# Optimization experiments

Hardware: AMD Instinct MI355X
Metric: run time of the kernel (lower is better)

The kernel has to match this reference:

```python
import jax, jax.numpy as jnp
import numpy as np

DT = 0.5
T = 50

def rho(x):
    return jnp.clip(x, 0.0, 1.0)

def rhop(x):
    return ((x >= 0.0) & (x <= 1.0)).astype(x.dtype)

def setup_inputs() -> dict:
    key = jax.random.key(0)
    ks = jax.random.split(key, 8)
    B, OUT, H, IN = 16384, 10, 256, 784
    data = jax.random.uniform(ks[0], (B, IN), dtype=jnp.float32)
    s0 = jnp.zeros((B, OUT), jnp.float32)
    s1 = jnp.zeros((B, H), jnp.float32)
    s2 = jnp.zeros((B, H), jnp.float32)
    # nn.Linear weights: shape (out_features, in_features), y = x @ W.T + b
    def lin(k, o, i):
        bound = 1.0 / np.sqrt(i)
        kw, kb = jax.random.split(k)
        W = jax.random.uniform(kw, (o, i), jnp.float32, -bound, bound)
        b = jax.random.uniform(kb, (o,), jnp.float32, -bound, bound)
        return W, b
    W0, b0 = lin(ks[1], OUT, H)   # w[0]: Linear(H, OUT)
    W2, b2 = lin(ks[2], H, H)     # w[2]: Linear(H, H)
    W4, b4 = lin(ks[3], H, IN)    # w[-1]: Linear(IN, H)
    return {"data": data, "s0": s0, "s1": s1, "s2": s2,
            "W0": W0, "b0": b0, "W2": W2, "b2": b2, "W4": W4, "b4": b4}

def reference(data, s0, s1, s2, W0, b0, W2, b2, W4, b4):
    # method='nograd', beta=0: run T stepper iterations, clamp states to [0,1].
    rdata = rho(data)  # constant over time steps
    def step(s, _):
        s0, s1, s2 = s
        d0 = -s0 + rho(s1) @ W0.T + b0
        d1 = -s1 + rhop(s1) * (rho(s2) @ W2.T + b2 + rho(s0) @ W0)
        d2 = -s2 + rhop(s2) * (rdata @ W4.T + b4 + rho(s1) @ W2)
        s0 = jnp.clip(s0 + DT * d0, 0.0, 1.0)
        s1 = jnp.clip(s1 + DT * d1, 0.0, 1.0)
        s2 = jnp.clip(s2 + DT * d2, 0.0, 1.0)
        return (s0, s1, s2), None
    (s0, s1, s2), _ = jax.lax.scan(step, (s0, s1, s2), None, length=T)
    return (s0, s1, s2)
```

## Files before the change

kernel.cpp:

```cpp
#include <hip/hip_runtime.h>

typedef _Float16 f16;
typedef _Float16 f16x8 __attribute__((ext_vector_type(8)));
typedef _Float16 f16x4 __attribute__((ext_vector_type(4)));
typedef float f32x4 __attribute__((ext_vector_type(4)));

#define MFMA16(a, b, c) __builtin_amdgcn_mfma_f32_16x16x32_f16((a), (b), (c), 0, 0, 0)
#define CLAMP01(x) __builtin_amdgcn_fmed3f((x), 0.0f, 1.0f)

constexpr int BATCH = 16384;
constexpr int H     = 256;
constexpr int IN    = 784;
constexpr int OUT   = 10;
constexpr int TSTEP = 50;
constexpr int BM    = 64;
constexpr int NTHR  = 512;
constexpr int SROW  = 264;
constexpr int S0ROW = 40;
constexpr int DROW  = 808;
constexpr int BXROW = 268;
constexpr int W0TROW= 16;
constexpr int EROW  = 268;

constexpr int OFF_S1  = 0;
constexpr int OFF_S2  = OFF_S1 + BM * SROW;
constexpr int OFF_S0  = OFF_S2 + BM * SROW;
constexpr int OFF_W0N = OFF_S0 + BM * S0ROW;
constexpr int OFF_W0T = OFF_W0N + 16 * SROW;
constexpr int OFF_B2  = OFF_W0T + H * W0TROW;
constexpr int OFF_BX  = OFF_B2 + 2 * H;
constexpr int POOL_F16 = OFF_BX + 2 * BM * BXROW;

__global__ __launch_bounds__(NTHR, 2) void ep_step_kernel(
    const float* __restrict__ data, const float* __restrict__ s0_in,
    const float* __restrict__ s1_in, const float* __restrict__ s2_in,
    const float* __restrict__ W0, const float* __restrict__ b0,
    const float* __restrict__ W2, const float* __restrict__ b2,
    const float* __restrict__ W4, const float* __restrict__ b4,
    float* __restrict__ out)
{
    __shared__ __align__(16) f16 pool[POOL_F16];

    const int tid  = threadIdx.x;
    const int wave = tid >> 6;
    const int lane = tid & 63;
    const int q    = lane >> 4;
    const int l16  = lane & 15;
    const int m0   = blockIdx.x * BM;
    const bool isS1 = (wave >= 4);
    const int  dmt  = wave & 3;
    const int h0   = (wave & 3) * 64;
    const int hx   = wave * 32;

    float* const bx  = (float*)&pool[OFF_BX];
    float* const b2l = (float*)&pool[OFF_B2];

    for (int i = tid; i < BM * (DROW / 4); i += NTHR) {
        int m  = i / (DROW / 4);
        int k4 = (i % (DROW / 4)) * 4;
        f16x4 p = {(f16)0.f, (f16)0.f, (f16)0.f, (f16)0.f};
        if (k4 < IN) {
            f32x4 v = *(const f32x4*)(data + (size_t)(m0 + m) * IN + k4);
            #pragma unroll
            for (int j = 0; j < 4; ++j) p[j] = (f16)CLAMP01(v[j]);
        }
        *(f16x4*)&pool[m * DROW + k4] = p;
    }
    __syncthreads();

    f32x4 x2a[2][4] = {};
    for (int kk = 0; kk < 25; ++kk) {
        int kb = kk * 32 + q * 8;
        f16x8 bd[4];
        #pragma unroll
        for (int mt = 0; mt < 4; ++mt)
            bd[mt] = *(const f16x8*)&pool[(mt * 16 + l16) * DROW + kb];
        #pragma unroll
        for (int ht = 0; ht < 2; ++ht) {
            int h = hx + ht * 16 + l16;
            f16x8 wa4;
            if (kk < 24) {
                f32x4 u0 = *(const f32x4*)(W4 + (size_t)h * IN + kb);
                f32x4 u1 = *(const f32x4*)(W4 + (size_t)h * IN + kb + 4);
                #pragma unroll
                for (int j = 0; j < 4; ++j) { wa4[j] = (f16)u0[j]; wa4[j + 4] = (f16)u1[j]; }
            } else {
                #pragma unroll
                for (int j = 0; j < 8; ++j) {
                    int k = kb + j;
                    wa4[j] = (k < IN) ? (f16)W4[(size_t)h * IN + k] : (f16)0.f;
                }
            }
            #pragma unroll
            for (int mt = 0; mt < 4; ++mt)
                x2a[ht][mt] = MFMA16(wa4, bd[mt], x2a[ht][mt]);
        }
    }
    __syncthreads();

    #pragma unroll
    for (int ht = 0; ht < 2; ++ht)
        #pragma unroll
        for (int mt = 0; mt < 4; ++mt) {
            f32x4 v = x2a[ht][mt];
            #pragma unroll
            for (int r = 0; r < 4; ++r) v[r] = 0.5f * (v[r] + b4[hx + ht * 16 + q * 4 + r]);
            *(f32x4*)&bx[(mt * 16 + l16) * BXROW + hx + ht * 16 + q * 4] = v;
        }
    for (int i = tid; i < 16 * SROW; i += NTHR) {
        int o = i / SROW, k = i % SROW;
        pool[OFF_W0N + i] = (o < OUT && k < H) ? (f16)W0[o * H + k] : (f16)0.f;
    }
    for (int i = tid; i < H * W0TROW; i += NTHR) {
        int h = i / W0TROW, o = i % W0TROW;
        pool[OFF_W0T + i] = (o < OUT) ? (f16)W0[o * H + h] : (f16)0.f;
    }
    for (int i = tid; i < H; i += NTHR) b2l[i] = 0.5f * b2[i];
    for (int i = tid; i < BM * S0ROW; i += NTHR) pool[OFF_S0 + i] = (f16)0.f;
    __syncthreads();

    asm volatile("" ::: "memory");
    f16x8 w[4][8];
    if (!isS1) {
        #pragma unroll
        for (int ht = 0; ht < 4; ++ht) {
            int h = h0 + ht * 16 + l16;
            #pragma unroll
            for (int kk = 0; kk < 8; ++kk) {
                int kb = kk * 32 + q * 8;
                f16x8 wa;
                #pragma unroll
                for (int j = 0; j < 8; ++j) wa[j] = (f16)W2[(kb + j) * H + h];
                w[ht][kk] = wa;
            }
        }
    } else {
        #pragma unroll
        for (int ht = 0; ht < 4; ++ht) {
            int h = h0 + ht * 16 + l16;
            #pragma unroll
            for (int kk = 0; kk < 8; ++kk) {
                int kb = kk * 32 + q * 8;
                f32x4 u0 = *(const f32x4*)(W2 + h * H + kb);
                f32x4 u1 = *(const f32x4*)(W2 + h * H + kb + 4);
                f16x8 wb;
                #pragma unroll
                for (int j = 0; j < 4; ++j) { wb[j] = (f16)u0[j]; wb[j + 4] = (f16)u1[j]; }
                w[ht][kk] = wb;
            }
        }
    }
    f32x4 sm[4][4];
    const float* sin_p = isS1 ? s1_in : s2_in;
    #pragma unroll
    for (int ht = 0; ht < 4; ++ht)
        #pragma unroll
        for (int mt = 0; mt < 4; ++mt)
            sm[ht][mt] = *(const f32x4*)&sin_p[(size_t)(m0 + mt * 16 + l16) * H + h0 + ht * 16 + q * 4];
    f32x4 s0m = {0.f, 0.f, 0.f, 0.f}, b0h = {0.f, 0.f, 0.f, 0.f};
    if (!isS1) {
        #pragma unroll
        for (int r = 0; r < 4; ++r) {
            int o = q * 4 + r;
            if (o < OUT) {
                s0m[r] = s0_in[(size_t)(m0 + dmt * 16 + l16) * OUT + o];
                b0h[r] = 0.5f * b0[o];
            }
        }
    }

    auto writeback = [&]() {
        f16* ws = &pool[isS1 ? OFF_S1 : OFF_S2];
        #pragma unroll
        for (int ht = 0; ht < 4; ++ht) {
            int hb = h0 + ht * 16 + q * 4;
            #pragma unroll
            for (int mt = 0; mt < 4; ++mt) {
                f16x4 p;
                #pragma unroll
                for (int r = 0; r < 4; ++r) p[r] = (f16)sm[ht][mt][r];
                *(f16x4*)&ws[(mt * 16 + l16) * SROW + hb] = p;
            }
        }
        if (!isS1) {
            int ob = q * 4;
            if (ob < OUT) {
                f16x4 p;
                #pragma unroll
                for (int r = 0; r < 4; ++r) p[r] = (ob + r < OUT) ? (f16)s0m[r] : (f16)0.f;
                *(f16x4*)&pool[OFF_S0 + (dmt * 16 + l16) * S0ROW + ob] = p;
            }
        }
    };

    auto compute = [&]() {
        const f16* rs = &pool[isS1 ? OFF_S2 : OFF_S1];
        if (isS1) {
            #pragma unroll
            for (int ht = 0; ht < 4; ++ht) {
                f16x8 w0cv = {};
                if (q < 2)
                    w0cv = *(const f16x8*)&pool[OFF_W0T + (h0 + ht * 16 + l16) * W0TROW + q * 8];
                #pragma unroll
                for (int mt = 0; mt < 4; ++mt) {
                    f16x8 b0v = *(const f16x8*)&pool[OFF_S0 + (mt * 16 + l16) * S0ROW + q * 8];
                    sm[ht][mt] = MFMA16(w0cv, b0v, sm[ht][mt]);
                }
            }
        }
        #pragma unroll
        for (int kk = 0; kk < 8; ++kk) {
            int kb = kk * 32 + q * 8;
            f16x8 b[4];
            #pragma unroll
            for (int mt = 0; mt < 4; ++mt)
                b[mt] = *(const f16x8*)&rs[(mt * 16 + l16) * SROW + kb];
            #pragma unroll
            for (int ht = 0; ht < 4; ++ht)
                #pragma unroll
                for (int mt = 0; mt < 4; ++mt)
                    sm[ht][mt] = MFMA16(w[ht][kk], b[mt], sm[ht][mt]);
            if (!isS1) {
                f16x8 a0 = *(const f16x8*)&pool[OFF_W0N + l16 * SROW + kb];
                #pragma unroll
                for (int mt = 0; mt < 4; ++mt)
                    if (mt == dmt) s0m = MFMA16(a0, b[mt], s0m);
            }
        }
        if (isS1) {
            #pragma unroll
            for (int ht = 0; ht < 4; ++ht) {
                f32x4 bhv = *(const f32x4*)&b2l[h0 + ht * 16 + q * 4];
                #pragma unroll
                for (int mt = 0; mt < 4; ++mt)
                    #pragma unroll
                    for (int r = 0; r < 4; ++r)
                        sm[ht][mt][r] = CLAMP01(fmaf(0.5f, sm[ht][mt][r], bhv[r]));
            }
        } else {
            #pragma unroll
            for (int ht = 0; ht < 4; ++ht)
                #pragma unroll
                for (int mt = 0; mt < 4; ++mt) {
                    f32x4 bv = *(const f32x4*)&bx[(mt * 16 + l16) * BXROW + h0 + ht * 16 + q * 4];
                    #pragma unroll
                    for (int r = 0; r < 4; ++r)
                        sm[ht][mt][r] = CLAMP01(fmaf(0.5f, sm[ht][mt][r], bv[r]));
                }
            #pragma unroll
            for (int r = 0; r < 4; ++r)
                s0m[r] = CLAMP01(fmaf(0.5f, s0m[r], b0h[r]));
        }
    };

    writeback();
    __syncthreads();

    #pragma unroll 1
    for (int t = 0; t < TSTEP; ++t) {
        compute();
        __syncthreads();
        writeback();
        __syncthreads();
    }

    if (!isS1) {
        #pragma unroll
        for (int r = 0; r < 4; ++r) {
            int o = q * 4 + r;
            if (o < OUT) out[(size_t)(m0 + dmt * 16 + l16) * OUT + o] = s0m[r];
        }
    }
    float* xf = (float*)pool;
    float* o1p = out + (size_t)BATCH * OUT;
    float* o2p = o1p + (size_t)BATCH * H;
    if (isS1) {
        #pragma unroll
        for (int ht = 0; ht < 4; ++ht)
            #pragma unroll
            for (int mt = 0; mt < 4; ++mt)
                *(f32x4*)&xf[(mt * 16 + l16) * EROW + h0 + ht * 16 + q * 4] = sm[ht][mt];
    }
    __syncthreads();
    for (int i = tid; i < BM * H / 4; i += NTHR) {
        int m = i >> 6, c = (i & 63) * 4;
        f32x4 v = *(const f32x4*)&xf[m * EROW + c];
        *(f32x4*)&o1p[(size_t)(m0 + m) * H + c] = v;
    }
    __syncthreads();
    if (!isS1) {
        #pragma unroll
        for (int ht = 0; ht < 4; ++ht)
            #pragma unroll
            for (int mt = 0; mt < 4; ++mt)
                *(f32x4*)&xf[(mt * 16 + l16) * EROW + h0 + ht * 16 + q * 4] = sm[ht][mt];
    }
    __syncthreads();
    for (int i = tid; i < BM * H / 4; i += NTHR) {
        int m = i >> 6, c = (i & 63) * 4;
        f32x4 v = *(const f32x4*)&xf[m * EROW + c];
        *(f32x4*)&o2p[(size_t)(m0 + m) * H + c] = v;
    }
}

extern "C" void kernel_launch(void* const* d_in, const int* in_sizes, int n_in,
                              void* d_out, int out_size, void* d_ws, size_t ws_size,
                              hipStream_t stream) {
    const float* data  = (const float*)d_in[0];
    const float* s0_in = (const float*)d_in[1];
    const float* s1_in = (const float*)d_in[2];
    const float* s2_in = (const float*)d_in[3];
    const float* W0    = (const float*)d_in[4];
    const float* b0    = (const float*)d_in[5];
    const float* W2    = (const float*)d_in[6];
    const float* b2    = (const float*)d_in[7];
    const float* W4    = (const float*)d_in[8];
    const float* b4    = (const float*)d_in[9];
    float* out = (float*)d_out;

    ep_step_kernel<<<BATCH / BM, NTHR, 0, stream>>>(
        data, s0_in, s1_in, s2_in, W0, b0, W2, b2, W4, b4, out);
}
```

Before: 383.1 us.

## Double waves per block, halving per-wave hidden tile and register footprint

Raises the block from 8 to 16 waves, so each wave owns 32 hidden columns instead of 64. This halves the register-resident W2 slice and accumulators and asks for 4 waves per SIMD. The output-layer work is kept on one even wave per batch tile. The aim is more latency hiding and parallel MFMA issue per CU in the serial time loop. In exchange, each block-wide barrier now covers more waves, and every wave still loads the full B-operand tiles from LDS, so LDS read traffic per step doubles.

```diff
diff --git a/kernel.cpp b/kernel.cpp
--- a/kernel.cpp
+++ b/kernel.cpp
@@ -14,7 +14,7 @@
 constexpr int OUT   = 10;
 constexpr int TSTEP = 50;
 constexpr int BM    = 64;
-constexpr int NTHR  = 512;
+constexpr int NTHR  = 1024;
 constexpr int SROW  = 264;
 constexpr int S0ROW = 40;
 constexpr int DROW  = 808;
@@ -31,7 +31,7 @@
 constexpr int OFF_BX  = OFF_B2 + 2 * H;
 constexpr int POOL_F16 = OFF_BX + 2 * BM * BXROW;
 
-__global__ __launch_bounds__(NTHR, 2) void ep_step_kernel(
+__global__ __launch_bounds__(NTHR, 4) void ep_step_kernel(
     const float* __restrict__ data, const float* __restrict__ s0_in,
     const float* __restrict__ s1_in, const float* __restrict__ s2_in,
     const float* __restrict__ W0, const float* __restrict__ b0,
@@ -47,10 +47,11 @@
     const int q    = lane >> 4;
     const int l16  = lane & 15;
     const int m0   = blockIdx.x * BM;
-    const bool isS1 = (wave >= 4);
-    const int  dmt  = wave & 3;
-    const int h0   = (wave & 3) * 64;
-    const int hx   = wave * 32;
+    const bool isS1 = (wave >= 8);
+    const bool duty = (!isS1 && (wave & 1) == 0);
+    const int  dmt  = wave >> 1;
+    const int h0   = (wave & 7) * 32;
+    const int hx   = wave * 16;
 
     float* const bx  = (float*)&pool[OFF_BX];
     float* const b2l = (float*)&pool[OFF_B2];
@@ -68,45 +69,40 @@
     }
     __syncthreads();
 
-    f32x4 x2a[2][4] = {};
+    f32x4 x2a[4] = {};
     for (int kk = 0; kk < 25; ++kk) {
         int kb = kk * 32 + q * 8;
         f16x8 bd[4];
         #pragma unroll
         for (int mt = 0; mt < 4; ++mt)
             bd[mt] = *(const f16x8*)&pool[(mt * 16 + l16) * DROW + kb];
-        #pragma unroll
-        for (int ht = 0; ht < 2; ++ht) {
-            int h = hx + ht * 16 + l16;
-            f16x8 wa4;
-            if (kk < 24) {
-                f32x4 u0 = *(const f32x4*)(W4 + (size_t)h * IN + kb);
-                f32x4 u1 = *(const f32x4*)(W4 + (size_t)h * IN + kb + 4);
-                #pragma unroll
-                for (int j = 0; j < 4; ++j) { wa4[j] = (f16)u0[j]; wa4[j + 4] = (f16)u1[j]; }
-            } else {
-                #pragma unroll
-                for (int j = 0; j < 8; ++j) {
-                    int k = kb + j;
-                    wa4[j] = (k < IN) ? (f16)W4[(size_t)h * IN + k] : (f16)0.f;
-                }
-            }
-            #pragma unroll
-            for (int mt = 0; mt < 4; ++mt)
-                x2a[ht][mt] = MFMA16(wa4, bd[mt], x2a[ht][mt]);
-        }
+        int h = hx + l16;
+        f16x8 wa4;
+        if (kk < 24) {
+            f32x4 u0 = *(const f32x4*)(W4 + (size_t)h * IN + kb);
+            f32x4 u1 = *(const f32x4*)(W4 + (size_t)h * IN + kb + 4);
+            #pragma unroll
+            for (int j = 0; j < 4; ++j) { wa4[j] = (f16)u0[j]; wa4[j + 4] = (f16)u1[j]; }
+        } else {
+            #pragma unroll
+            for (int j = 0; j < 8; ++j) {
+                int k = kb + j;
+                wa4[j] = (k < IN) ? (f16)W4[(size_t)h * IN + k] : (f16)0.f;
+            }
+        }
+        #pragma unroll
+        for (int mt = 0; mt < 4; ++mt)
+            x2a[mt] = MFMA16(wa4, bd[mt], x2a[mt]);
     }
     __syncthreads();
 
     #pragma unroll
-    for (int ht = 0; ht < 2; ++ht)
-        #pragma unroll
-        for (int mt = 0; mt < 4; ++mt) {
-            f32x4 v = x2a[ht][mt];
-            #pragma unroll
-            for (int r = 0; r < 4; ++r) v[r] = 0.5f * (v[r] + b4[hx + ht * 16 + q * 4 + r]);
-            *(f32x4*)&bx[(mt * 16 + l16) * BXROW + hx + ht * 16 + q * 4] = v;
-        }
+    for (int mt = 0; mt < 4; ++mt) {
+        f32x4 v = x2a[mt];
+        #pragma unroll
+        for (int r = 0; r < 4; ++r) v[r] = 0.5f * (v[r] + b4[hx + q * 4 + r]);
+        *(f32x4*)&bx[(mt * 16 + l16) * BXROW + hx + q * 4] = v;
+    }
     for (int i = tid; i < 16 * SROW; i += NTHR) {
         int o = i / SROW, k = i % SROW;
         pool[OFF_W0N + i] = (o < OUT && k < H) ? (f16)W0[o * H + k] : (f16)0.f;
@@ -120,10 +116,10 @@
     __syncthreads();
 
     asm volatile("" ::: "memory");
-    f16x8 w[4][8];
+    f16x8 w[2][8];
     if (!isS1) {
         #pragma unroll
-        for (int ht = 0; ht < 4; ++ht) {
+        for (int ht = 0; ht < 2; ++ht) {
             int h = h0 + ht * 16 + l16;
             #pragma unroll
             for (int kk = 0; kk < 8; ++kk) {
@@ -136,7 +132,7 @@
         }
     } else {
         #pragma unroll
-        for (int ht = 0; ht < 4; ++ht) {
+        for (int ht = 0; ht < 2; ++ht) {
             int h = h0 + ht * 16 + l16;
             #pragma unroll
             for (int kk = 0; kk < 8; ++kk) {
@@ -150,15 +146,15 @@
             }
         }
     }
-    f32x4 sm[4][4];
+    f32x4 sm[2][4];
     const float* sin_p = isS1 ? s1_in : s2_in;
     #pragma unroll
-    for (int ht = 0; ht < 4; ++ht)
+    for (int ht = 0; ht < 2; ++ht)
         #pragma unroll
         for (int mt = 0; mt < 4; ++mt)
             sm[ht][mt] = *(const f32x4*)&sin_p[(size_t)(m0 + mt * 16 + l16) * H + h0 + ht * 16 + q * 4];
     f32x4 s0m = {0.f, 0.f, 0.f, 0.f}, b0h = {0.f, 0.f, 0.f, 0.f};
-    if (!isS1) {
+    if (duty) {
         #pragma unroll
         for (int r = 0; r < 4; ++r) {
             int o = q * 4 + r;
@@ -172,7 +168,7 @@
     auto writeback = [&]() {
         f16* ws = &pool[isS1 ? OFF_S1 : OFF_S2];
         #pragma unroll
-        for (int ht = 0; ht < 4; ++ht) {
+        for (int ht = 0; ht < 2; ++ht) {
             int hb = h0 + ht * 16 + q * 4;
             #pragma unroll
             for (int mt = 0; mt < 4; ++mt) {
@@ -182,7 +178,7 @@
                 *(f16x4*)&ws[(mt * 16 + l16) * SROW + hb] = p;
             }
         }
-        if (!isS1) {
+        if (duty) {
             int ob = q * 4;
             if (ob < OUT) {
                 f16x4 p;
@@ -197,7 +193,7 @@
         const f16* rs = &pool[isS1 ? OFF_S2 : OFF_S1];
         if (isS1) {
             #pragma unroll
-            for (int ht = 0; ht < 4; ++ht) {
+            for (int ht = 0; ht < 2; ++ht) {
                 f16x8 w0cv = {};
                 if (q < 2)
                     w0cv = *(const f16x8*)&pool[OFF_W0T + (h0 + ht * 16 + l16) * W0TROW + q * 8];
@@ -211,25 +207,28 @@
         #pragma unroll
         for (int kk = 0; kk < 8; ++kk) {
             int kb = kk * 32 + q * 8;
-            f16x8 b[4];
-            #pragma unroll
-            for (int mt = 0; mt < 4; ++mt)
-                b[mt] = *(const f16x8*)&rs[(mt * 16 + l16) * SROW + kb];
-            #pragma unroll
-            for (int ht = 0; ht < 4; ++ht)
-                #pragma unroll
-                for (int mt = 0; mt < 4; ++mt)
-                    sm[ht][mt] = MFMA16(w[ht][kk], b[mt], sm[ht][mt]);
-            if (!isS1) {
-                f16x8 a0 = *(const f16x8*)&pool[OFF_W0N + l16 * SROW + kb];
-                #pragma unroll
-                for (int mt = 0; mt < 4; ++mt)
-                    if (mt == dmt) s0m = MFMA16(a0, b[mt], s0m);
+            #pragma unroll
+            for (int mp = 0; mp < 2; ++mp) {
+                f16x8 bA = *(const f16x8*)&rs[((mp * 2 + 0) * 16 + l16) * SROW + kb];
+                f16x8 bB = *(const f16x8*)&rs[((mp * 2 + 1) * 16 + l16) * SROW + kb];
+                sm[0][mp * 2 + 0] = MFMA16(w[0][kk], bA, sm[0][mp * 2 + 0]);
+                sm[1][mp * 2 + 0] = MFMA16(w[1][kk], bA, sm[1][mp * 2 + 0]);
+                sm[0][mp * 2 + 1] = MFMA16(w[0][kk], bB, sm[0][mp * 2 + 1]);
+                sm[1][mp * 2 + 1] = MFMA16(w[1][kk], bB, sm[1][mp * 2 + 1]);
+                if (duty) {
+                    if (dmt == mp * 2 + 0) {
+                        f16x8 a0 = *(const f16x8*)&pool[OFF_W0N + l16 * SROW + kb];
+                        s0m = MFMA16(a0, bA, s0m);
+                    } else if (dmt == mp * 2 + 1) {
+                        f16x8 a0 = *(const f16x8*)&pool[OFF_W0N + l16 * SROW + kb];
+                        s0m = MFMA16(a0, bB, s0m);
+                    }
+                }
             }
         }
         if (isS1) {
             #pragma unroll
-            for (int ht = 0; ht < 4; ++ht) {
+            for (int ht = 0; ht < 2; ++ht) {
                 f32x4 bhv = *(const f32x4*)&b2l[h0 + ht * 16 + q * 4];
                 #pragma unroll
                 for (int mt = 0; mt < 4; ++mt)
@@ -239,7 +238,7 @@
             }
         } else {
             #pragma unroll
-            for (int ht = 0; ht < 4; ++ht)
+            for (int ht = 0; ht < 2; ++ht)
                 #pragma unroll
                 for (int mt = 0; mt < 4; ++mt) {
                     f32x4 bv = *(const f32x4*)&bx[(mt * 16 + l16) * BXROW + h0 + ht * 16 + q * 4];
@@ -247,9 +246,11 @@
                     for (int r = 0; r < 4; ++r)
                         sm[ht][mt][r] = CLAMP01(fmaf(0.5f, sm[ht][mt][r], bv[r]));
                 }
-            #pragma unroll
-            for (int r = 0; r < 4; ++r)
-                s0m[r] = CLAMP01(fmaf(0.5f, s0m[r], b0h[r]));
+            if (duty) {
+                #pragma unroll
+                for (int r = 0; r < 4; ++r)
+                    s0m[r] = CLAMP01(fmaf(0.5f, s0m[r], b0h[r]));
+            }
         }
     };
 
@@ -264,7 +265,7 @@
         __syncthreads();
     }
 
-    if (!isS1) {
+    if (duty) {
         #pragma unroll
         for (int r = 0; r < 4; ++r) {
             int o = q * 4 + r;
@@ -276,7 +277,7 @@
     float* o2p = o1p + (size_t)BATCH * H;
     if (isS1) {
         #pragma unroll
-        for (int ht = 0; ht < 4; ++ht)
+        for (int ht = 0; ht < 2; ++ht)
             #pragma unroll
             for (int mt = 0; mt < 4; ++mt)
                 *(f32x4*)&xf[(mt * 16 + l16) * EROW + h0 + ht * 16 + q * 4] = sm[ht][mt];
@@ -290,7 +291,7 @@
     __syncthreads();
     if (!isS1) {
         #pragma unroll
-        for (int ht = 0; ht < 4; ++ht)
+        for (int ht = 0; ht < 2; ++ht)
             #pragma unroll
             for (int mt = 0; mt < 4; ++mt)
                 *(f32x4*)&xf[(mt * 16 + l16) * EROW + h0 + ht * 16 + q * 4] = sm[ht][mt];
```

Measured after the change: 392.3 us. 2.4% more time.

## Double-buffer state tiles in LDS and move bias stash to global scratch

Applied to the files above, without the earlier changes.

The s1/s2/s0 state tiles in shared memory are double-buffered, so each time step needs one barrier instead of two: compute reads one set while writeback fills the other. To free LDS for the second buffer, the per-row data bias (W4·x + b4) is moved to a scratch area in the global output buffer and re-read every step with software prefetch. The transposed W0 tile is now held in registers. The extra global reads per step and higher register pressure may offset the saved barrier, and reusing the output region as scratch depends on the final writes overwriting it.

```diff
diff --git a/kernel.cpp b/kernel.cpp
--- a/kernel.cpp
+++ b/kernel.cpp
@@ -18,18 +18,15 @@
 constexpr int SROW  = 264;
 constexpr int S0ROW = 40;
 constexpr int DROW  = 808;
-constexpr int BXROW = 268;
-constexpr int W0TROW= 16;
 constexpr int EROW  = 268;
 
+constexpr int SBUF    = BM * SROW;
 constexpr int OFF_S1  = 0;
-constexpr int OFF_S2  = OFF_S1 + BM * SROW;
-constexpr int OFF_S0  = OFF_S2 + BM * SROW;
-constexpr int OFF_W0N = OFF_S0 + BM * S0ROW;
-constexpr int OFF_W0T = OFF_W0N + 16 * SROW;
-constexpr int OFF_B2  = OFF_W0T + H * W0TROW;
-constexpr int OFF_BX  = OFF_B2 + 2 * H;
-constexpr int POOL_F16 = OFF_BX + 2 * BM * BXROW;
+constexpr int OFF_S2  = 2 * SBUF;
+constexpr int OFF_S0  = 4 * SBUF;
+constexpr int OFF_W0N = OFF_S0 + 2 * BM * S0ROW;
+constexpr int OFF_B2  = OFF_W0N + 16 * SROW;
+constexpr int POOL_F16 = OFF_B2 + 2 * H;
 
 __global__ __launch_bounds__(NTHR, 2) void ep_step_kernel(
     const float* __restrict__ data, const float* __restrict__ s0_in,
@@ -52,8 +49,8 @@
     const int h0   = (wave & 3) * 64;
     const int hx   = wave * 32;
 
-    float* const bx  = (float*)&pool[OFF_BX];
     float* const b2l = (float*)&pool[OFF_B2];
+    float* const biasg = out + (size_t)BATCH * OUT + (size_t)BATCH * H;
 
     for (int i = tid; i < BM * (DROW / 4); i += NTHR) {
         int m  = i / (DROW / 4);
@@ -105,22 +102,19 @@
             f32x4 v = x2a[ht][mt];
             #pragma unroll
             for (int r = 0; r < 4; ++r) v[r] = 0.5f * (v[r] + b4[hx + ht * 16 + q * 4 + r]);
-            *(f32x4*)&bx[(mt * 16 + l16) * BXROW + hx + ht * 16 + q * 4] = v;
+            *(f32x4*)&biasg[(size_t)(m0 + mt * 16 + l16) * H + hx + ht * 16 + q * 4] = v;
         }
     for (int i = tid; i < 16 * SROW; i += NTHR) {
         int o = i / SROW, k = i % SROW;
         pool[OFF_W0N + i] = (o < OUT && k < H) ? (f16)W0[o * H + k] : (f16)0.f;
     }
-    for (int i = tid; i < H * W0TROW; i += NTHR) {
-        int h = i / W0TROW, o = i % W0TROW;
-        pool[OFF_W0T + i] = (o < OUT) ? (f16)W0[o * H + h] : (f16)0.f;
-    }
     for (int i = tid; i < H; i += NTHR) b2l[i] = 0.5f * b2[i];
-    for (int i = tid; i < BM * S0ROW; i += NTHR) pool[OFF_S0 + i] = (f16)0.f;
+    for (int i = tid; i < 2 * BM * S0ROW; i += NTHR) pool[OFF_S0 + i] = (f16)0.f;
     __syncthreads();
 
     asm volatile("" ::: "memory");
     f16x8 w[4][8];
+    f16x8 w0c[4];
     if (!isS1) {
         #pragma unroll
         for (int ht = 0; ht < 4; ++ht) {
@@ -148,6 +142,11 @@
                 for (int j = 0; j < 4; ++j) { wb[j] = (f16)u0[j]; wb[j + 4] = (f16)u1[j]; }
                 w[ht][kk] = wb;
             }
+            #pragma unroll
+            for (int j = 0; j < 8; ++j) {
+                int o = q * 8 + j;
+                w0c[ht][j] = (o < OUT) ? (f16)W0[o * H + h] : (f16)0.f;
+            }
         }
     }
     f32x4 sm[4][4];
@@ -169,8 +168,8 @@
         }
     }
 
-    auto writeback = [&]() {
-        f16* ws = &pool[isS1 ? OFF_S1 : OFF_S2];
+    auto writeback = [&](int set) {
+        f16* ws = &pool[(isS1 ? OFF_S1 : OFF_S2) + set * SBUF];
         #pragma unroll
         for (int ht = 0; ht < 4; ++ht) {
             int hb = h0 + ht * 16 + q * 4;
@@ -188,25 +187,24 @@
                 f16x4 p;
                 #pragma unroll
                 for (int r = 0; r < 4; ++r) p[r] = (ob + r < OUT) ? (f16)s0m[r] : (f16)0.f;
-                *(f16x4*)&pool[OFF_S0 + (dmt * 16 + l16) * S0ROW + ob] = p;
+                *(f16x4*)&pool[OFF_S0 + set * BM * S0ROW + (dmt * 16 + l16) * S0ROW + ob] = p;
             }
         }
     };
 
-    auto compute = [&]() {
-        const f16* rs = &pool[isS1 ? OFF_S2 : OFF_S1];
+    auto compute = [&](int set) {
+        const f16* rs  = &pool[(isS1 ? OFF_S2 : OFF_S1) + set * SBUF];
+        const f16* rs0 = &pool[OFF_S0 + set * BM * S0ROW];
         if (isS1) {
-            #pragma unroll
-            for (int ht = 0; ht < 4; ++ht) {
-                f16x8 w0cv = {};
-                if (q < 2)
-                    w0cv = *(const f16x8*)&pool[OFF_W0T + (h0 + ht * 16 + l16) * W0TROW + q * 8];
-                #pragma unroll
-                for (int mt = 0; mt < 4; ++mt) {
-                    f16x8 b0v = *(const f16x8*)&pool[OFF_S0 + (mt * 16 + l16) * S0ROW + q * 8];
-                    sm[ht][mt] = MFMA16(w0cv, b0v, sm[ht][mt]);
-                }
-            }
+            f16x8 b0v[4];
+            #pragma unroll
+            for (int mt = 0; mt < 4; ++mt)
+                b0v[mt] = *(const f16x8*)&rs0[(mt * 16 + l16) * S0ROW + q * 8];
+            #pragma unroll
+            for (int ht = 0; ht < 4; ++ht)
+                #pragma unroll
+                for (int mt = 0; mt < 4; ++mt)
+                    sm[ht][mt] = MFMA16(w0c[ht], b0v[mt], sm[ht][mt]);
         }
         #pragma unroll
         for (int kk = 0; kk < 8; ++kk) {
@@ -238,30 +236,41 @@
                         sm[ht][mt][r] = CLAMP01(fmaf(0.5f, sm[ht][mt][r], bhv[r]));
             }
         } else {
-            #pragma unroll
-            for (int ht = 0; ht < 4; ++ht)
-                #pragma unroll
-                for (int mt = 0; mt < 4; ++mt) {
-                    f32x4 bv = *(const f32x4*)&bx[(mt * 16 + l16) * BXROW + h0 + ht * 16 + q * 4];
+            f32x4 bcur[4], bnext[4];
+            #pragma unroll
+            for (int mt = 0; mt < 4; ++mt)
+                bcur[mt] = *(const f32x4*)&biasg[(size_t)(m0 + mt * 16 + l16) * H + h0 + q * 4];
+            #pragma unroll
+            for (int ht = 0; ht < 4; ++ht) {
+                if (ht < 3)
+                    #pragma unroll
+                    for (int mt = 0; mt < 4; ++mt)
+                        bnext[mt] = *(const f32x4*)&biasg[(size_t)(m0 + mt * 16 + l16) * H
+                                                          + h0 + (ht + 1) * 16 + q * 4];
+                #pragma unroll
+                for (int mt = 0; mt < 4; ++mt)
                     #pragma unroll
                     for (int r = 0; r < 4; ++r)
-                        sm[ht][mt][r] = CLAMP01(fmaf(0.5f, sm[ht][mt][r], bv[r]));
-                }
+                        sm[ht][mt][r] = CLAMP01(fmaf(0.5f, sm[ht][mt][r], bcur[mt][r]));
+                #pragma unroll
+                for (int mt = 0; mt < 4; ++mt) bcur[mt] = bnext[mt];
+            }
             #pragma unroll
             for (int r = 0; r < 4; ++r)
                 s0m[r] = CLAMP01(fmaf(0.5f, s0m[r], b0h[r]));
         }
     };
 
-    writeback();
-    __syncthreads();
-
+    writeback(0);
+    __syncthreads();
+
+    int cur = 0;
     #pragma unroll 1
     for (int t = 0; t < TSTEP; ++t) {
-        compute();
+        compute(cur);
+        writeback(cur ^ 1);
         __syncthreads();
-        writeback();
-        __syncthreads();
+        cur ^= 1;
     }
 
     if (!isS1) {
```

Measured after the change: 679.4 us. +77.4%, slower.
